# Performance work log

Hardware: AMD Instinct MI355X
Metric: run time of the kernel (lower is better)

## Reference

```python
import math
import jax, jax.numpy as jnp
import numpy as np

B, H, W, C = 4, 64, 64, 96
SSM_RATIO = 2.0
D_INNER = int(SSM_RATIO * C)   # 192
D_STATE = 4
DT_RANK = math.ceil(C / 16)    # 6
K = 4                          # 4 scan directions
D_CONV = 3


def layer_norm(x, g, b, eps=1e-5):
    mu = jnp.mean(x, axis=-1, keepdims=True)
    var = jnp.var(x, axis=-1, keepdims=True)
    return (x - mu) / jnp.sqrt(var + eps) * g + b


def cross_scan(x):
    # x: (B, D, H, W) -> (B, K=4, D, L); dirs: row-major, col-major, and their reverses
    b, d, h, w = x.shape
    s0 = x.reshape(b, d, h * w)
    s1 = jnp.transpose(x, (0, 1, 3, 2)).reshape(b, d, h * w)
    return jnp.stack([s0, s1, s0[..., ::-1], s1[..., ::-1]], axis=1)


def cross_merge(ys, h, w):
    # ys: (B, K=4, D, L) -> (B, D, L); inverse of cross_scan, summed over directions
    b, k, d, L = ys.shape
    ys = ys[:, 0:2] + ys[:, 2:4][..., ::-1]
    y0 = ys[:, 0]
    y1 = jnp.transpose(ys[:, 1].reshape(b, d, w, h), (0, 1, 3, 2)).reshape(b, d, L)
    return y0 + y1


def selective_scan(u, dt, A, Bm, Cm, D4):
    # u, dt: (B,K,D,L); A: (K,D,N); Bm, Cm: (B,K,N,L); D4: (K,D)
    u_l = jnp.moveaxis(u, -1, 0)    # (L,B,K,D)
    dt_l = jnp.moveaxis(dt, -1, 0)
    B_l = jnp.moveaxis(Bm, -1, 0)   # (L,B,K,N)
    C_l = jnp.moveaxis(Cm, -1, 0)

    def step(h, inp):
        u_t, dt_t, B_t, C_t = inp
        dA = jnp.exp(dt_t[..., None] * A)                              # (B,K,D,N)
        h = h * dA + dt_t[..., None] * B_t[:, :, None, :] * u_t[..., None]
        y = jnp.sum(h * C_t[:, :, None, :], axis=-1)                   # (B,K,D)
        return h, y

    h0 = jnp.zeros(u.shape[:3] + (A.shape[-1],), u.dtype)
    _, ys = jax.lax.scan(step, h0, (u_l, dt_l, B_l, C_l))
    return jnp.moveaxis(ys, 0, -1) + D4[None, :, :, None] * u


def _block(x_rgb, x_e, in_proj_x_w, in_proj_e_w, conv_x_w, conv_x_b, conv_e_w, conv_e_b,
           x_proj_weight, dt_projs_weight, dt_projs_bias, A_logs, Ds,
           ln_r_g, ln_r_b, ln_e_g, ln_e_b, out_proj_x_w, out_proj_e_w):
    b, h, w, c = x_rgb.shape
    Din, N, R = D_INNER, D_STATE, DT_RANK

    xr = jnp.einsum('bhwc,dc->bhwd', x_rgb, in_proj_x_w)
    xe = jnp.einsum('bhwc,dc->bhwd', x_e, in_proj_e_w)
    xr = jnp.transpose(xr, (0, 3, 1, 2))  # (B,Din,H,W)
    xe = jnp.transpose(xe, (0, 3, 1, 2))

    def dwconv(x, wt, bias):
        y = jax.lax.conv_general_dilated(x, wt, (1, 1), 'SAME', feature_group_count=Din)
        return jax.nn.silu(y + bias[None, :, None, None])

    xr = dwconv(xr, conv_x_w, conv_x_b)
    xe = dwconv(xe, conv_e_w, conv_e_b)

    xs_r = cross_scan(xr)  # (B,K,Din,L)
    xs_e = cross_scan(xe)

    def proj(xs):
        dbl = jnp.einsum('bkdl,kcd->bkcl', xs, x_proj_weight)
        dtl, Bm, Cm = dbl[:, :, :R], dbl[:, :, R:R + N], dbl[:, :, R + N:]
        dtl = jnp.einsum('bkrl,kdr->bkdl', dtl, dt_projs_weight)
        dtl = jax.nn.softplus(dtl + dt_projs_bias[None, :, :, None])
        return dtl, Bm, Cm

    dt_r, B_r, C_r = proj(xs_r)
    dt_e, B_e, C_e = proj(xs_e)

    A = -jnp.exp(A_logs).reshape(K, Din, N)
    D4 = Ds.reshape(K, Din)

    # cross fusion: each modality's scan reads out through the OTHER modality's C
    y_r = selective_scan(xs_r, dt_r, A, B_r, C_e, D4)
    y_e = selective_scan(xs_e, dt_e, A, B_e, C_r, D4)

    y_r = cross_merge(y_r, h, w)  # (B,Din,L)
    y_e = cross_merge(y_e, h, w)

    y_r = layer_norm(jnp.transpose(y_r, (0, 2, 1)), ln_r_g, ln_r_b).reshape(b, h, w, Din)
    y_e = layer_norm(jnp.transpose(y_e, (0, 2, 1)), ln_e_g, ln_e_b).reshape(b, h, w, Din)

    out_r = jnp.einsum('bhwd,cd->bhwc', y_r, out_proj_x_w)
    out_e = jnp.einsum('bhwd,cd->bhwc', y_e, out_proj_e_w)

    # residual add of the wrapping block (drop_path=0, mlp_ratio=0)
    return x_rgb + out_r, x_e + out_e


def setup_inputs():
    key = jax.random.key(0)
    ks = jax.random.split(key, 16)
    N, R, Din = D_STATE, DT_RANK, D_INNER

    def rn(k, shape, s=0.02):
        return (jax.random.normal(k, shape) * s).astype(jnp.float32)

    # dt bias: inverse-softplus of dt ~ U[1e-3, 0.1]  (mamba-style init)
    dt = jnp.exp(jax.random.uniform(ks[10], (K, Din)) * (np.log(0.1) - np.log(1e-3)) + np.log(1e-3))
    dt_bias = dt + jnp.log(-jnp.expm1(-dt))

    return {
        'x_rgb': jax.random.normal(ks[0], (B, H, W, C), jnp.float32),
        'x_e': jax.random.normal(ks[1], (B, H, W, C), jnp.float32),
        'in_proj_x_w': rn(ks[2], (Din, C)),
        'in_proj_e_w': rn(ks[3], (Din, C)),
        'conv_x_w': rn(ks[4], (Din, 1, D_CONV, D_CONV), 0.1),
        'conv_x_b': jnp.zeros((Din,), jnp.float32),
        'conv_e_w': rn(ks[5], (Din, 1, D_CONV, D_CONV), 0.1),
        'conv_e_b': jnp.zeros((Din,), jnp.float32),
        'x_proj_weight': rn(ks[6], (K, R + 2 * N, Din)),
        'dt_projs_weight': rn(ks[7], (K, Din, R), R ** -0.5),
        'dt_projs_bias': dt_bias.astype(jnp.float32),
        'A_logs': jnp.log(jnp.tile(jnp.arange(1, N + 1, dtype=jnp.float32), (K * Din, 1))),
        'Ds': jnp.ones((K * Din,), jnp.float32),
        'ln_r_g': jnp.ones((Din,), jnp.float32),
        'ln_r_b': jnp.zeros((Din,), jnp.float32),
        'ln_e_g': jnp.ones((Din,), jnp.float32),
        'ln_e_b': jnp.zeros((Din,), jnp.float32),
        'out_proj_x_w': rn(ks[8], (C, Din)),
        'out_proj_e_w': rn(ks[9], (C, Din)),
    }


def reference(x_rgb, x_e, in_proj_x_w, in_proj_e_w, conv_x_w, conv_x_b, conv_e_w, conv_e_b,
              x_proj_weight, dt_projs_weight, dt_projs_bias, A_logs, Ds,
              ln_r_g, ln_r_b, ln_e_g, ln_e_b, out_proj_x_w, out_proj_e_w):
    return _block(x_rgb, x_e, in_proj_x_w, in_proj_e_w, conv_x_w, conv_x_b, conv_e_w, conv_e_b,
                  x_proj_weight, dt_projs_weight, dt_projs_bias, A_logs, Ds,
                  ln_r_g, ln_r_b, ln_e_g, ln_e_b, out_proj_x_w, out_proj_e_w)
```

## Files before the change

kernel.cpp:

```cpp
#include <hip/hip_runtime.h>

#define BB 4
#define HH 64
#define WW 64
#define CC 96
#define DIN 192
#define NS 4
#define RR 6
#define KK 4
#define LL 4096
#define NPOS (BB*LL)
#define NPD ((size_t)NPOS*DIN)
#define NDBC ((size_t)BB*KK*LL*14)
#define NCHUNK 128
#define CLEN 32
#define NCHAIN 32
#define PB 16
#define TP 16

__device__ __forceinline__ int map_pos(int k, int l){
  switch(k){
    case 0: return l;
    case 1: { int wi=l>>6, hi=l&63; return hi*WW+wi; }
    case 2: return LL-1-l;
    default:{ int lr=LL-1-l; int wi=lr>>6, hi=lr&63; return hi*WW+wi; }
  }
}
__device__ __forceinline__ int pos_stride(int k){
  return (k==0) ? 1 : (k==1) ? WW : (k==2) ? -1 : -WW;
}

__global__ __launch_bounds__(DIN) void inproj_kernel(
    const float* __restrict__ x_rgb, const float* __restrict__ x_e,
    const float* __restrict__ w_r,   const float* __restrict__ w_e,
    float* __restrict__ xproj_r,    float* __restrict__ xproj_e){
  int blk = blockIdx.x;
  int m = blk / (NPOS/PB); int g = blk % (NPOS/PB);
  size_t rem0 = (size_t)g * PB;
  const float* x = m ? x_e : x_rgb;
  const float* w = m ? w_e : w_r;
  float* o = m ? xproj_e : xproj_r;
  __shared__ float4 xs4[PB*24];
  __shared__ float4 wt4[DIN*5];
  int t = threadIdx.x;

  const float4* xg = (const float4*)(x + rem0*CC);
  xs4[t]       = xg[t];
  xs4[t + 192] = xg[t + 192];

  float acc[PB];
  #pragma unroll
  for(int p=0;p<PB;p++) acc[p]=0.f;

  for(int c0=0; c0<CC; c0+=16){
    __syncthreads();
    const float* wr = w + (size_t)t*CC + c0;
    wt4[t*5+0] = *(const float4*)(wr);
    wt4[t*5+1] = *(const float4*)(wr+4);
    wt4[t*5+2] = *(const float4*)(wr+8);
    wt4[t*5+3] = *(const float4*)(wr+12);
    __syncthreads();
    int cq0 = c0 >> 2;
    #pragma unroll
    for(int q=0;q<4;q++){
      float4 w4 = wt4[t*5+q];
      #pragma unroll
      for(int p=0;p<PB;p++){
        float4 x4 = xs4[p*24 + cq0 + q];
        acc[p] = fmaf(x4.x,w4.x, fmaf(x4.y,w4.y, fmaf(x4.z,w4.z, fmaf(x4.w,w4.w, acc[p]))));
      }
    }
  }
  #pragma unroll
  for(int p=0;p<PB;p++) o[(rem0+p)*DIN + t] = acc[p];
}

__global__ __launch_bounds__(DIN) void conv_kernel(
    const float* __restrict__ xproj_r, const float* __restrict__ xproj_e,
    const float* __restrict__ cw_r, const float* __restrict__ cb_r,
    const float* __restrict__ cw_e, const float* __restrict__ cb_e,
    float* __restrict__ xconv_r, float* __restrict__ xconv_e){
  int blk = blockIdx.x;
  int m = blk / NPOS; int rem = blk % NPOS;
  int b = rem / LL, p = rem % LL;
  int y = p >> 6, x = p & 63;
  const float* in = (m ? xproj_e : xproj_r) + (size_t)b*LL*DIN;
  const float* cw = m ? cw_e : cw_r;
  const float* cb = m ? cb_e : cb_r;
  float* out = m ? xconv_e : xconv_r;
  int d = threadIdx.x;
  float acc = cb[d];
  #pragma unroll
  for(int dy=-1;dy<=1;dy++){
    int yy = y+dy; if(yy<0 || yy>=HH) continue;
    #pragma unroll
    for(int dx=-1;dx<=1;dx++){
      int xx = x+dx; if(xx<0 || xx>=WW) continue;
      acc += in[(size_t)(yy*WW+xx)*DIN + d] * cw[d*9 + (dy+1)*3 + (dx+1)];
    }
  }
  float s = acc / (1.f + __expf(-acc));
  out[(size_t)(b*LL+p)*DIN + d] = s;
}

#define TPOS 32
__global__ __launch_bounds__(256) void projbc_kernel(
    const float* __restrict__ xconv_r, const float* __restrict__ xconv_e,
    const float* __restrict__ xpw,
    float* __restrict__ dtBC_r, float* __restrict__ dtBC_e){
  int blk = blockIdx.x;
  int m = blk / (BB*LL/TPOS); int rem = blk % (BB*LL/TPOS);
  int b = rem / (LL/TPOS); int p0 = (rem % (LL/TPOS)) * TPOS;
  const float* xc = (m ? xconv_e : xconv_r) + ((size_t)b*LL + p0)*DIN;
  float* o = (m ? dtBC_e : dtBC_r) + (size_t)b*KK*LL*14;

  __shared__ float xs[TPOS*97];
  __shared__ float wsd[56*97];

  int t = threadIdx.x;
  int g = t >> 5;
  int pl = t & 31;

  float acc[7];
  #pragma unroll
  for(int j=0;j<7;j++) acc[j]=0.f;

  for(int dt0=0; dt0<DIN; dt0+=96){
    __syncthreads();
    for(int idx=t; idx<TPOS*96; idx+=256){
      int r = idx/96, ccol = idx%96;
      xs[r*97+ccol] = xc[(size_t)r*DIN + dt0 + ccol];
    }
    for(int idx=t; idx<56*96; idx+=256){
      int r = idx/96, ccol = idx%96;
      wsd[r*97+ccol] = xpw[(size_t)r*DIN + dt0 + ccol];
    }
    __syncthreads();
    const float* xrow = &xs[pl*97];
    #pragma unroll 4
    for(int d=0; d<96; d++){
      float xv = xrow[d];
      #pragma unroll
      for(int j=0;j<7;j++) acc[j] += wsd[(g*7+j)*97 + d]*xv;
    }
  }

  int p = p0 + pl;
  int ptr_ = (p&63)*64 + (p>>6);
  #pragma unroll
  for(int j=0;j<7;j++){
    int cbar = g*7+j;
    int k = cbar/14, c = cbar%14;
    int l = (k==0) ? p : (k==1) ? ptr_ : (k==2) ? (LL-1-p) : (LL-1-ptr_);
    o[((size_t)k*LL + l)*14 + c] = acc[j];
  }
}

__global__ __launch_bounds__(DIN) void scan_p1_kernel(
    const float* __restrict__ xconv_r, const float* __restrict__ xconv_e,
    const float* __restrict__ dtBC_r, const float* __restrict__ dtBC_e,
    const float* __restrict__ dtw, const float* __restrict__ dtb,
    const float* __restrict__ A_logs,
    float* __restrict__ trans_S, float* __restrict__ sumdt){
  int ch = blockIdx.x / NCHUNK;
  int cidx = blockIdx.x % NCHUNK;
  int m = ch >> 4, b = (ch>>2)&3, k = ch&3;
  int d = threadIdx.x;
  int l0 = cidx*CLEN;

  float4 al = *(const float4*)&A_logs[(size_t)(k*DIN+d)*NS];
  float A0=-__expf(al.x), A1=-__expf(al.y), A2=-__expf(al.z), A3=-__expf(al.w);
  float Wd[RR];
  #pragma unroll
  for(int r=0;r<RR;r++) Wd[r] = dtw[((size_t)k*DIN + d)*RR + r];
  float bias = dtb[k*DIN+d];

  const float* xc    = (m ? xconv_e : xconv_r) + (size_t)b*LL*DIN;
  const float* dbc_m = (m ? dtBC_e : dtBC_r) + ((size_t)b*KK + k)*LL*14;

  __shared__ float4 db4[CLEN][4];
  __shared__ float u_s[CLEN*DIN];
  float* dbf = (float*)db4;

  for(int idx=d; idx<CLEN*14; idx+=DIN){
    int i = idx/14, j = idx%14;
    int slot = (j<6) ? (8+j) : (j-6);
    dbf[i*16+slot] = dbc_m[(size_t)l0*14 + idx];
  }
  int stride = pos_stride(k);
  int pos0 = map_pos(k, l0);
  #pragma unroll 8
  for(int i=0;i<CLEN;i++)
    u_s[i*DIN+d] = xc[(size_t)(pos0+i*stride)*DIN + d];
  __syncthreads();

  float h0=0.f,h1=0.f,h2=0.f,h3=0.f,sd=0.f;
  #pragma unroll 4
  for(int i=0;i<CLEN;i++){
    float4 Bv  = db4[i][0];
    float4 d03 = db4[i][2];
    float4 d45 = db4[i][3];
    float dtr = fmaf(d03.x,Wd[0], fmaf(d03.y,Wd[1], fmaf(d03.z,Wd[2],
                fmaf(d03.w,Wd[3], fmaf(d45.x,Wd[4], fmaf(d45.y,Wd[5], bias))))));
    float dt = fmaxf(dtr,0.f) + __logf(1.f + __expf(-fabsf(dtr)));
    sd += dt;
    float u = u_s[i*DIN + d];
    float dtu = dt*u;
    h0 = fmaf(h0, __expf(dt*A0), dtu*Bv.x);
    h1 = fmaf(h1, __expf(dt*A1), dtu*Bv.y);
    h2 = fmaf(h2, __expf(dt*A2), dtu*Bv.z);
    h3 = fmaf(h3, __expf(dt*A3), dtu*Bv.w);
  }
  size_t base = ((size_t)(ch*NCHUNK + cidx)*NS)*DIN + d;
  trans_S[base          ] = h0;
  trans_S[base +   DIN  ] = h1;
  trans_S[base + 2*DIN  ] = h2;
  trans_S[base + 3*DIN  ] = h3;
  sumdt[(size_t)(ch*NCHUNK + cidx)*DIN + d] = sd;
}

__global__ __launch_bounds__(DIN) void scan_p2_kernel(
    const float* __restrict__ trans_S, const float* __restrict__ sumdt,
    const float* __restrict__ A_logs, float* __restrict__ hin){
  int ch = blockIdx.x; int k = ch & 3; int d = threadIdx.x;
  float4 al = *(const float4*)&A_logs[(size_t)(k*DIN+d)*NS];
  float A[NS] = {-__expf(al.x), -__expf(al.y), -__expf(al.z), -__expf(al.w)};
  float h[NS] = {0.f,0.f,0.f,0.f};
  for(int c0=0;c0<NCHUNK;c0+=4){
    float S[4][NS], sdv[4];
    #pragma unroll
    for(int cc=0;cc<4;cc++){
      size_t base = ((size_t)(ch*NCHUNK + c0+cc)*NS)*DIN + d;
      #pragma unroll
      for(int n=0;n<NS;n++) S[cc][n] = trans_S[base + (size_t)n*DIN];
      sdv[cc] = sumdt[(size_t)(ch*NCHUNK + c0+cc)*DIN + d];
    }
    #pragma unroll
    for(int cc=0;cc<4;cc++){
      size_t base = ((size_t)(ch*NCHUNK + c0+cc)*NS)*DIN + d;
      #pragma unroll
      for(int n=0;n<NS;n++) hin[base + (size_t)n*DIN] = h[n];
      #pragma unroll
      for(int n=0;n<NS;n++) h[n] = fmaf(h[n], __expf(A[n]*sdv[cc]), S[cc][n]);
    }
  }
}

__global__ __launch_bounds__(DIN) void scan_p3_kernel(
    const float* __restrict__ xconv_r, const float* __restrict__ xconv_e,
    const float* __restrict__ dtBC_r, const float* __restrict__ dtBC_e,
    const float* __restrict__ dtw, const float* __restrict__ dtb,
    const float* __restrict__ A_logs, const float* __restrict__ Ds,
    const float* __restrict__ hin,
    float* __restrict__ ym_a_r, float* __restrict__ ym_a_e,
    float* __restrict__ ym_b_r, float* __restrict__ ym_b_e){
  int blk = blockIdx.x;
  int cidx = blk % NCHUNK;
  int rem  = blk / NCHUNK;
  int pg = rem & 1; rem >>= 1;
  int b  = rem & 3; int m = rem >> 2;
  int kA = pg, kB = pg + 2;
  int cidx2 = NCHUNK-1-cidx;
  int l0A = cidx*CLEN, l0B = cidx2*CLEN;

  int d = threadIdx.x;
  int st = pos_stride(kA);
  int pos0 = map_pos(kA, l0A);

  const float* xc = (m ? xconv_e : xconv_r) + (size_t)b*LL*DIN;
  const float* dbc_own = (m ? dtBC_e : dtBC_r) + (size_t)b*KK*LL*14;
  const float* dbc_oth = (m ? dtBC_r : dtBC_e) + (size_t)b*KK*LL*14;
  float* ym = (pg==0) ? (m ? ym_a_e : ym_a_r) : (m ? ym_b_e : ym_b_r);
  ym += (size_t)b*LL*DIN;

  __shared__ float4 db4A[CLEN][4];
  __shared__ float4 db4B[CLEN][4];
  __shared__ float u_s[CLEN*DIN];
  float* dbfA = (float*)db4A;
  float* dbfB = (float*)db4B;

  for(int idx=d; idx<CLEN*14; idx+=DIN){
    int i = idx/14, j = idx%14;
    int slot = (j<6) ? (8+j) : (j-6);
    dbfA[i*16+slot] = dbc_own[((size_t)kA*LL + l0A)*14 + idx];
    dbfB[i*16+slot] = dbc_own[((size_t)kB*LL + l0B)*14 + idx];
  }
  for(int idx=d; idx<CLEN*NS; idx+=DIN){
    int i = idx>>2, j = idx&3;
    dbfA[i*16 + 4 + j] = dbc_oth[((size_t)kA*LL + l0A + i)*14 + 10 + j];
    dbfB[i*16 + 4 + j] = dbc_oth[((size_t)kB*LL + l0B + i)*14 + 10 + j];
  }
  #pragma unroll 8
  for(int i=0;i<CLEN;i++)
    u_s[i*DIN+d] = xc[(size_t)(pos0+i*st)*DIN + d];
  __syncthreads();

  {
    int k = kA;
    float4 al = *(const float4*)&A_logs[(size_t)(k*DIN+d)*NS];
    float A0=-__expf(al.x), A1=-__expf(al.y), A2=-__expf(al.z), A3=-__expf(al.w);
    float Wd[RR];
    #pragma unroll
    for(int r=0;r<RR;r++) Wd[r] = dtw[((size_t)k*DIN + d)*RR + r];
    float bias = dtb[k*DIN+d];
    float Dv = Ds[k*DIN+d];
    int chA = (m*4+b)*4 + kA;
    size_t hbase = ((size_t)(chA*NCHUNK + cidx)*NS)*DIN + d;
    float h0=hin[hbase], h1=hin[hbase+DIN], h2=hin[hbase+2*DIN], h3=hin[hbase+3*DIN];
    #pragma unroll 4
    for(int i=0;i<CLEN;i++){
      float4 Bv  = db4A[i][0];
      float4 Cv  = db4A[i][1];
      float4 d03 = db4A[i][2];
      float4 d45 = db4A[i][3];
      float dtr = fmaf(d03.x,Wd[0], fmaf(d03.y,Wd[1], fmaf(d03.z,Wd[2],
                  fmaf(d03.w,Wd[3], fmaf(d45.x,Wd[4], fmaf(d45.y,Wd[5], bias))))));
      float dt = fmaxf(dtr,0.f) + __logf(1.f + __expf(-fabsf(dtr)));
      float u = u_s[i*DIN + d];
      float dtu = dt*u;
      h0 = fmaf(h0, __expf(dt*A0), dtu*Bv.x);
      h1 = fmaf(h1, __expf(dt*A1), dtu*Bv.y);
      h2 = fmaf(h2, __expf(dt*A2), dtu*Bv.z);
      h3 = fmaf(h3, __expf(dt*A3), dtu*Bv.w);
      float y = fmaf(h0,Cv.x, fmaf(h1,Cv.y, fmaf(h2,Cv.z, fmaf(h3,Cv.w, Dv*u))));
      ym[(size_t)(pos0+i*st)*DIN + d] = y;
    }
  }
  {
    int k = kB;
    float4 al = *(const float4*)&A_logs[(size_t)(k*DIN+d)*NS];
    float A0=-__expf(al.x), A1=-__expf(al.y), A2=-__expf(al.z), A3=-__expf(al.w);
    float Wd[RR];
    #pragma unroll
    for(int r=0;r<RR;r++) Wd[r] = dtw[((size_t)k*DIN + d)*RR + r];
    float bias = dtb[k*DIN+d];
    float Dv = Ds[k*DIN+d];
    int chB = (m*4+b)*4 + kB;
    size_t hbase = ((size_t)(chB*NCHUNK + cidx2)*NS)*DIN + d;
    float h0=hin[hbase], h1=hin[hbase+DIN], h2=hin[hbase+2*DIN], h3=hin[hbase+3*DIN];
    #pragma unroll 4
    for(int j=0;j<CLEN;j++){
      int pi = CLEN-1-j;
      float4 Bv  = db4B[j][0];
      float4 Cv  = db4B[j][1];
      float4 d03 = db4B[j][2];
      float4 d45 = db4B[j][3];
      float dtr = fmaf(d03.x,Wd[0], fmaf(d03.y,Wd[1], fmaf(d03.z,Wd[2],
                  fmaf(d03.w,Wd[3], fmaf(d45.x,Wd[4], fmaf(d45.y,Wd[5], bias))))));
      float dt = fmaxf(dtr,0.f) + __logf(1.f + __expf(-fabsf(dtr)));
      float u = u_s[pi*DIN + d];
      float dtu = dt*u;
      h0 = fmaf(h0, __expf(dt*A0), dtu*Bv.x);
      h1 = fmaf(h1, __expf(dt*A1), dtu*Bv.y);
      h2 = fmaf(h2, __expf(dt*A2), dtu*Bv.z);
      h3 = fmaf(h3, __expf(dt*A3), dtu*Bv.w);
      float y = fmaf(h0,Cv.x, fmaf(h1,Cv.y, fmaf(h2,Cv.z, fmaf(h3,Cv.w, Dv*u))));
      size_t a = (size_t)(pos0+pi*st)*DIN + d;
      ym[a] += y;
    }
  }
}

__global__ __launch_bounds__(256) void ln_out_kernel(
    const float* __restrict__ ym_a_r, const float* __restrict__ ym_a_e,
    const float* __restrict__ ym_b_r, const float* __restrict__ ym_b_e,
    const float* __restrict__ ln_rg, const float* __restrict__ ln_rb,
    const float* __restrict__ ln_eg, const float* __restrict__ ln_eb,
    const float* __restrict__ opw_r, const float* __restrict__ opw_e,
    const float* __restrict__ x_rgb, const float* __restrict__ x_e,
    float* __restrict__ out){
  int blk = blockIdx.x;
  int m = blk / (NPOS/TP); int g = blk % (NPOS/TP);
  size_t rem0 = (size_t)g * TP;
  int t = threadIdx.x;

  __shared__ float yn_t[DIN][20];
  __shared__ float wt[CC][20];

  {
    int tp = t >> 4, j = t & 15;
    const float* yma = (m ? ym_a_e : ym_a_r) + (rem0+tp)*DIN;
    const float* ymb = (m ? ym_b_e : ym_b_r) + (rem0+tp)*DIN;
    float4 v4[3]; float s=0.f, q=0.f;
    #pragma unroll
    for(int e=0;e<3;e++){
      float4 a4 = *(const float4*)&yma[j*12 + e*4];
      float4 b4 = *(const float4*)&ymb[j*12 + e*4];
      v4[e] = make_float4(a4.x+b4.x, a4.y+b4.y, a4.z+b4.z, a4.w+b4.w);
      s += v4[e].x+v4[e].y+v4[e].z+v4[e].w;
      q += v4[e].x*v4[e].x + v4[e].y*v4[e].y + v4[e].z*v4[e].z + v4[e].w*v4[e].w;
    }
    #pragma unroll
    for(int off=8; off>0; off>>=1){ s += __shfl_xor(s,off); q += __shfl_xor(q,off); }
    float mu  = s*(1.f/DIN);
    float var = q*(1.f/DIN) - mu*mu;
    float inv = rsqrtf(var + 1e-5f);
    const float* gg = m ? ln_eg : ln_rg;
    const float* be = m ? ln_eb : ln_rb;
    #pragma unroll
    for(int e=0;e<3;e++){
      int dd = j*12 + e*4;
      float4 g4 = *(const float4*)&gg[dd];
      float4 b4 = *(const float4*)&be[dd];
      yn_t[dd+0][tp] = (v4[e].x-mu)*inv*g4.x + b4.x;
      yn_t[dd+1][tp] = (v4[e].y-mu)*inv*g4.y + b4.y;
      yn_t[dd+2][tp] = (v4[e].z-mu)*inv*g4.z + b4.z;
      yn_t[dd+3][tp] = (v4[e].w-mu)*inv*g4.w + b4.w;
    }
  }

  int c = t % CC;
  int pbase = t / CC;
  const float* w = (m ? opw_e : opw_r);
  float acc[8];
  #pragma unroll
  for(int pp=0;pp<8;pp++) acc[pp]=0.f;

  for(int d0=0; d0<DIN; d0+=16){
    __syncthreads();
    for(int idx=t; idx<CC*16; idx+=256){
      int r = idx>>4, cc2 = idx&15;
      wt[r][cc2] = w[(size_t)r*DIN + d0 + cc2];
    }
    __syncthreads();
    if(t < 192){
      #pragma unroll
      for(int q4=0; q4<4; q4++){
        float4 w4 = *(const float4*)&wt[c][q4*4];
        #pragma unroll
        for(int e=0;e<4;e++){
          int dd = d0 + q4*4 + e;
          float wv = (e==0)?w4.x:(e==1)?w4.y:(e==2)?w4.z:w4.w;
          float4 ylo = *(const float4*)&yn_t[dd][pbase*8];
          float4 yhi = *(const float4*)&yn_t[dd][pbase*8+4];
          acc[0] = fmaf(ylo.x, wv, acc[0]);
          acc[1] = fmaf(ylo.y, wv, acc[1]);
          acc[2] = fmaf(ylo.z, wv, acc[2]);
          acc[3] = fmaf(ylo.w, wv, acc[3]);
          acc[4] = fmaf(yhi.x, wv, acc[4]);
          acc[5] = fmaf(yhi.y, wv, acc[5]);
          acc[6] = fmaf(yhi.z, wv, acc[6]);
          acc[7] = fmaf(yhi.w, wv, acc[7]);
        }
      }
    }
  }
  if(t < 192){
    const float* xin = m ? x_e : x_rgb;
    #pragma unroll
    for(int pp=0;pp<8;pp++){
      size_t rem = rem0 + pbase*8 + pp;
      size_t oi = (size_t)m*NPOS*CC + rem*CC + c;
      out[oi] = acc[pp] + xin[rem*CC + c];
    }
  }
}

extern "C" void kernel_launch(void* const* d_in, const int* in_sizes, int n_in,
                              void* d_out, int out_size, void* d_ws, size_t ws_size,
                              hipStream_t stream){
  const float* x_rgb = (const float*)d_in[0];
  const float* x_e   = (const float*)d_in[1];
  const float* ipw_r = (const float*)d_in[2];
  const float* ipw_e = (const float*)d_in[3];
  const float* cw_r  = (const float*)d_in[4];
  const float* cb_r  = (const float*)d_in[5];
  const float* cw_e  = (const float*)d_in[6];
  const float* cb_e  = (const float*)d_in[7];
  const float* xpw   = (const float*)d_in[8];
  const float* dtw   = (const float*)d_in[9];
  const float* dtb   = (const float*)d_in[10];
  const float* Alog  = (const float*)d_in[11];
  const float* Ds_   = (const float*)d_in[12];
  const float* ln_rg = (const float*)d_in[13];
  const float* ln_rb = (const float*)d_in[14];
  const float* ln_eg = (const float*)d_in[15];
  const float* ln_eb = (const float*)d_in[16];
  const float* opw_r = (const float*)d_in[17];
  const float* opw_e = (const float*)d_in[18];
  float* out = (float*)d_out;

  float* ws = (float*)d_ws;
  float* xproj_r = ws;
  float* xproj_e = ws + NPD;
  float* xconv_r = ws + 2*NPD;
  float* xconv_e = ws + 3*NPD;
  float* dtBC_r  = ws + 4*NPD;
  float* dtBC_e  = ws + 4*NPD + NDBC;
  float* trans_S = ws + 4*NPD + 2*NDBC;
  float* sumdt   = trans_S + (size_t)NCHAIN*NCHUNK*NS*DIN;
  float* hin     = sumdt   + (size_t)NCHAIN*NCHUNK*DIN;
  float* ym_b_r  = hin     + (size_t)NCHAIN*NCHUNK*NS*DIN;
  float* ym_b_e  = ym_b_r + NPD;
  float* ym_a_r = xproj_r;
  float* ym_a_e = xproj_e;

  inproj_kernel<<<2*NPOS/PB, DIN, 0, stream>>>(x_rgb, x_e, ipw_r, ipw_e, xproj_r, xproj_e);
  conv_kernel<<<2*NPOS, DIN, 0, stream>>>(xproj_r, xproj_e, cw_r, cb_r, cw_e, cb_e, xconv_r, xconv_e);
  projbc_kernel<<<2*BB*(LL/TPOS), 256, 0, stream>>>(xconv_r, xconv_e, xpw, dtBC_r, dtBC_e);
  scan_p1_kernel<<<NCHAIN*NCHUNK, DIN, 0, stream>>>(xconv_r, xconv_e, dtBC_r, dtBC_e,
                                                    dtw, dtb, Alog, trans_S, sumdt);
  scan_p2_kernel<<<NCHAIN, DIN, 0, stream>>>(trans_S, sumdt, Alog, hin);
  scan_p3_kernel<<<2*BB*2*NCHUNK, DIN, 0, stream>>>(xconv_r, xconv_e, dtBC_r, dtBC_e,
                                                    dtw, dtb, Alog, Ds_, hin,
                                                    ym_a_r, ym_a_e, ym_b_r, ym_b_e);
  ln_out_kernel<<<2*NPOS/TP, 256, 0, stream>>>(ym_a_r, ym_a_e, ym_b_r, ym_b_e,
                                               ln_rg, ln_rb, ln_eg, ln_eb,
                                               opw_r, opw_e, x_rgb, x_e, out);
}
```

Before: 373.0 us.

## Pair forward/reverse scan directions in pass 1, buffer outputs, widen LN-out tile

Scan pass 1 now handles a direction and its reverse in one block, so the u chunk is loaded from global memory once for both. This halves the block count and the redundant xconv reads. Scan pass 3 keeps the forward outputs in a fully unrolled register array and writes each ym element once, removing the read-modify-write accumulation. The LayerNorm/out-projection kernel now processes 32 positions per block with 16 accumulators per thread, so weight tiles are reused more. The cost is higher register pressure (a 32-float array plus 16 accumulators), which may reduce occupancy.

Result: slower. 381.6 us (+2.3%).

```diff
diff --git a/kernel.cpp b/kernel.cpp
--- a/kernel.cpp
+++ b/kernel.cpp
@@ -16,7 +16,7 @@
 #define CLEN 32
 #define NCHAIN 32
 #define PB 16
-#define TP 16
+#define TP 32
 
 __device__ __forceinline__ int map_pos(int k, int l){
   switch(k){
@@ -162,61 +162,105 @@
     const float* __restrict__ dtw, const float* __restrict__ dtb,
     const float* __restrict__ A_logs,
     float* __restrict__ trans_S, float* __restrict__ sumdt){
-  int ch = blockIdx.x / NCHUNK;
-  int cidx = blockIdx.x % NCHUNK;
-  int m = ch >> 4, b = (ch>>2)&3, k = ch&3;
+  int blk = blockIdx.x;
+  int cidx = blk % NCHUNK;
+  int rem  = blk / NCHUNK;
+  int pg = rem & 1; rem >>= 1;
+  int b  = rem & 3; int m = rem >> 2;
+  int kA = pg, kB = pg + 2;
+  int cidx2 = NCHUNK-1-cidx;
+  int l0A = cidx*CLEN, l0B = cidx2*CLEN;
   int d = threadIdx.x;
-  int l0 = cidx*CLEN;
-
-  float4 al = *(const float4*)&A_logs[(size_t)(k*DIN+d)*NS];
-  float A0=-__expf(al.x), A1=-__expf(al.y), A2=-__expf(al.z), A3=-__expf(al.w);
-  float Wd[RR];
-  #pragma unroll
-  for(int r=0;r<RR;r++) Wd[r] = dtw[((size_t)k*DIN + d)*RR + r];
-  float bias = dtb[k*DIN+d];
-
-  const float* xc    = (m ? xconv_e : xconv_r) + (size_t)b*LL*DIN;
-  const float* dbc_m = (m ? dtBC_e : dtBC_r) + ((size_t)b*KK + k)*LL*14;
-
-  __shared__ float4 db4[CLEN][4];
+  int st = pos_stride(kA);
+  int pos0 = map_pos(kA, l0A);
+
+  const float* xc = (m ? xconv_e : xconv_r) + (size_t)b*LL*DIN;
+  const float* dbc_own = (m ? dtBC_e : dtBC_r) + (size_t)b*KK*LL*14;
+
+  __shared__ float4 db4A[CLEN][4];
+  __shared__ float4 db4B[CLEN][4];
   __shared__ float u_s[CLEN*DIN];
-  float* dbf = (float*)db4;
+  float* dbfA = (float*)db4A;
+  float* dbfB = (float*)db4B;
 
   for(int idx=d; idx<CLEN*14; idx+=DIN){
     int i = idx/14, j = idx%14;
     int slot = (j<6) ? (8+j) : (j-6);
-    dbf[i*16+slot] = dbc_m[(size_t)l0*14 + idx];
-  }
-  int stride = pos_stride(k);
-  int pos0 = map_pos(k, l0);
+    dbfA[i*16+slot] = dbc_own[((size_t)kA*LL + l0A)*14 + idx];
+    dbfB[i*16+slot] = dbc_own[((size_t)kB*LL + l0B)*14 + idx];
+  }
   #pragma unroll 8
   for(int i=0;i<CLEN;i++)
-    u_s[i*DIN+d] = xc[(size_t)(pos0+i*stride)*DIN + d];
+    u_s[i*DIN+d] = xc[(size_t)(pos0+i*st)*DIN + d];
   __syncthreads();
 
-  float h0=0.f,h1=0.f,h2=0.f,h3=0.f,sd=0.f;
-  #pragma unroll 4
-  for(int i=0;i<CLEN;i++){
-    float4 Bv  = db4[i][0];
-    float4 d03 = db4[i][2];
-    float4 d45 = db4[i][3];
-    float dtr = fmaf(d03.x,Wd[0], fmaf(d03.y,Wd[1], fmaf(d03.z,Wd[2],
-                fmaf(d03.w,Wd[3], fmaf(d45.x,Wd[4], fmaf(d45.y,Wd[5], bias))))));
-    float dt = fmaxf(dtr,0.f) + __logf(1.f + __expf(-fabsf(dtr)));
-    sd += dt;
-    float u = u_s[i*DIN + d];
-    float dtu = dt*u;
-    h0 = fmaf(h0, __expf(dt*A0), dtu*Bv.x);
-    h1 = fmaf(h1, __expf(dt*A1), dtu*Bv.y);
-    h2 = fmaf(h2, __expf(dt*A2), dtu*Bv.z);
-    h3 = fmaf(h3, __expf(dt*A3), dtu*Bv.w);
-  }
-  size_t base = ((size_t)(ch*NCHUNK + cidx)*NS)*DIN + d;
-  trans_S[base          ] = h0;
-  trans_S[base +   DIN  ] = h1;
-  trans_S[base + 2*DIN  ] = h2;
-  trans_S[base + 3*DIN  ] = h3;
-  sumdt[(size_t)(ch*NCHUNK + cidx)*DIN + d] = sd;
+  {
+    int k = kA;
+    float4 al = *(const float4*)&A_logs[(size_t)(k*DIN+d)*NS];
+    float A0=-__expf(al.x), A1=-__expf(al.y), A2=-__expf(al.z), A3=-__expf(al.w);
+    float Wd[RR];
+    #pragma unroll
+    for(int r=0;r<RR;r++) Wd[r] = dtw[((size_t)k*DIN + d)*RR + r];
+    float bias = dtb[k*DIN+d];
+    float h0=0.f,h1=0.f,h2=0.f,h3=0.f,sd=0.f;
+    #pragma unroll 4
+    for(int i=0;i<CLEN;i++){
+      float4 Bv  = db4A[i][0];
+      float4 d03 = db4A[i][2];
+      float4 d45 = db4A[i][3];
+      float dtr = fmaf(d03.x,Wd[0], fmaf(d03.y,Wd[1], fmaf(d03.z,Wd[2],
+                  fmaf(d03.w,Wd[3], fmaf(d45.x,Wd[4], fmaf(d45.y,Wd[5], bias))))));
+      float dt = fmaxf(dtr,0.f) + __logf(1.f + __expf(-fabsf(dtr)));
+      sd += dt;
+      float u = u_s[i*DIN + d];
+      float dtu = dt*u;
+      h0 = fmaf(h0, __expf(dt*A0), dtu*Bv.x);
+      h1 = fmaf(h1, __expf(dt*A1), dtu*Bv.y);
+      h2 = fmaf(h2, __expf(dt*A2), dtu*Bv.z);
+      h3 = fmaf(h3, __expf(dt*A3), dtu*Bv.w);
+    }
+    int chA = (m*4+b)*4 + kA;
+    size_t base = ((size_t)(chA*NCHUNK + cidx)*NS)*DIN + d;
+    trans_S[base        ] = h0;
+    trans_S[base +  DIN ] = h1;
+    trans_S[base + 2*DIN] = h2;
+    trans_S[base + 3*DIN] = h3;
+    sumdt[(size_t)(chA*NCHUNK + cidx)*DIN + d] = sd;
+  }
+  {
+    int k = kB;
+    float4 al = *(const float4*)&A_logs[(size_t)(k*DIN+d)*NS];
+    float A0=-__expf(al.x), A1=-__expf(al.y), A2=-__expf(al.z), A3=-__expf(al.w);
+    float Wd[RR];
+    #pragma unroll
+    for(int r=0;r<RR;r++) Wd[r] = dtw[((size_t)k*DIN + d)*RR + r];
+    float bias = dtb[k*DIN+d];
+    float h0=0.f,h1=0.f,h2=0.f,h3=0.f,sd=0.f;
+    #pragma unroll 4
+    for(int j=0;j<CLEN;j++){
+      int pi = CLEN-1-j;
+      float4 Bv  = db4B[j][0];
+      float4 d03 = db4B[j][2];
+      float4 d45 = db4B[j][3];
+      float dtr = fmaf(d03.x,Wd[0], fmaf(d03.y,Wd[1], fmaf(d03.z,Wd[2],
+                  fmaf(d03.w,Wd[3], fmaf(d45.x,Wd[4], fmaf(d45.y,Wd[5], bias))))));
+      float dt = fmaxf(dtr,0.f) + __logf(1.f + __expf(-fabsf(dtr)));
+      sd += dt;
+      float u = u_s[pi*DIN + d];
+      float dtu = dt*u;
+      h0 = fmaf(h0, __expf(dt*A0), dtu*Bv.x);
+      h1 = fmaf(h1, __expf(dt*A1), dtu*Bv.y);
+      h2 = fmaf(h2, __expf(dt*A2), dtu*Bv.z);
+      h3 = fmaf(h3, __expf(dt*A3), dtu*Bv.w);
+    }
+    int chB = (m*4+b)*4 + kB;
+    size_t base = ((size_t)(chB*NCHUNK + cidx2)*NS)*DIN + d;
+    trans_S[base        ] = h0;
+    trans_S[base +  DIN ] = h1;
+    trans_S[base + 2*DIN] = h2;
+    trans_S[base + 3*DIN] = h3;
+    sumdt[(size_t)(chB*NCHUNK + cidx2)*DIN + d] = sd;
+  }
 }
 
 __global__ __launch_bounds__(DIN) void scan_p2_kernel(
@@ -295,6 +339,8 @@
     u_s[i*DIN+d] = xc[(size_t)(pos0+i*st)*DIN + d];
   __syncthreads();
 
+  float yA[CLEN];
+
   {
     int k = kA;
     float4 al = *(const float4*)&A_logs[(size_t)(k*DIN+d)*NS];
@@ -307,7 +353,7 @@
     int chA = (m*4+b)*4 + kA;
     size_t hbase = ((size_t)(chA*NCHUNK + cidx)*NS)*DIN + d;
     float h0=hin[hbase], h1=hin[hbase+DIN], h2=hin[hbase+2*DIN], h3=hin[hbase+3*DIN];
-    #pragma unroll 4
+    #pragma unroll
     for(int i=0;i<CLEN;i++){
       float4 Bv  = db4A[i][0];
       float4 Cv  = db4A[i][1];
@@ -322,8 +368,7 @@
       h1 = fmaf(h1, __expf(dt*A1), dtu*Bv.y);
       h2 = fmaf(h2, __expf(dt*A2), dtu*Bv.z);
       h3 = fmaf(h3, __expf(dt*A3), dtu*Bv.w);
-      float y = fmaf(h0,Cv.x, fmaf(h1,Cv.y, fmaf(h2,Cv.z, fmaf(h3,Cv.w, Dv*u))));
-      ym[(size_t)(pos0+i*st)*DIN + d] = y;
+      yA[i] = fmaf(h0,Cv.x, fmaf(h1,Cv.y, fmaf(h2,Cv.z, fmaf(h3,Cv.w, Dv*u))));
     }
   }
   {
@@ -338,7 +383,7 @@
     int chB = (m*4+b)*4 + kB;
     size_t hbase = ((size_t)(chB*NCHUNK + cidx2)*NS)*DIN + d;
     float h0=hin[hbase], h1=hin[hbase+DIN], h2=hin[hbase+2*DIN], h3=hin[hbase+3*DIN];
-    #pragma unroll 4
+    #pragma unroll
     for(int j=0;j<CLEN;j++){
       int pi = CLEN-1-j;
       float4 Bv  = db4B[j][0];
@@ -355,8 +400,7 @@
       h2 = fmaf(h2, __expf(dt*A2), dtu*Bv.z);
       h3 = fmaf(h3, __expf(dt*A3), dtu*Bv.w);
       float y = fmaf(h0,Cv.x, fmaf(h1,Cv.y, fmaf(h2,Cv.z, fmaf(h3,Cv.w, Dv*u))));
-      size_t a = (size_t)(pos0+pi*st)*DIN + d;
-      ym[a] += y;
+      ym[(size_t)(pos0+pi*st)*DIN + d] = yA[pi] + y;
     }
   }
 }
@@ -374,32 +418,33 @@
   size_t rem0 = (size_t)g * TP;
   int t = threadIdx.x;
 
-  __shared__ float yn_t[DIN][20];
+  __shared__ float yn_t[DIN][36];
   __shared__ float wt[CC][20];
 
   {
-    int tp = t >> 4, j = t & 15;
+    int tp = t >> 3, j = t & 7;
     const float* yma = (m ? ym_a_e : ym_a_r) + (rem0+tp)*DIN;
     const float* ymb = (m ? ym_b_e : ym_b_r) + (rem0+tp)*DIN;
-    float4 v4[3]; float s=0.f, q=0.f;
-    #pragma unroll
-    for(int e=0;e<3;e++){
-      float4 a4 = *(const float4*)&yma[j*12 + e*4];
-      float4 b4 = *(const float4*)&ymb[j*12 + e*4];
+    float4 v4[6]; float s=0.f, q=0.f;
+    #pragma unroll
+    for(int e=0;e<6;e++){
+      int dd = j*4 + e*32;
+      float4 a4 = *(const float4*)&yma[dd];
+      float4 b4 = *(const float4*)&ymb[dd];
       v4[e] = make_float4(a4.x+b4.x, a4.y+b4.y, a4.z+b4.z, a4.w+b4.w);
       s += v4[e].x+v4[e].y+v4[e].z+v4[e].w;
       q += v4[e].x*v4[e].x + v4[e].y*v4[e].y + v4[e].z*v4[e].z + v4[e].w*v4[e].w;
     }
     #pragma unroll
-    for(int off=8; off>0; off>>=1){ s += __shfl_xor(s,off); q += __shfl_xor(q,off); }
+    for(int off=4; off>0; off>>=1){ s += __shfl_xor(s,off); q += __shfl_xor(q,off); }
     float mu  = s*(1.f/DIN);
     float var = q*(1.f/DIN) - mu*mu;
     float inv = rsqrtf(var + 1e-5f);
     const float* gg = m ? ln_eg : ln_rg;
     const float* be = m ? ln_eb : ln_rb;
     #pragma unroll
-    for(int e=0;e<3;e++){
-      int dd = j*12 + e*4;
+    for(int e=0;e<6;e++){
+      int dd = j*4 + e*32;
       float4 g4 = *(const float4*)&gg[dd];
       float4 b4 = *(const float4*)&be[dd];
       yn_t[dd+0][tp] = (v4[e].x-mu)*inv*g4.x + b4.x;
@@ -412,9 +457,9 @@
   int c = t % CC;
   int pbase = t / CC;
   const float* w = (m ? opw_e : opw_r);
-  float acc[8];
+  float acc[16];
   #pragma unroll
-  for(int pp=0;pp<8;pp++) acc[pp]=0.f;
+  for(int pp=0;pp<16;pp++) acc[pp]=0.f;
 
   for(int d0=0; d0<DIN; d0+=16){
     __syncthreads();
@@ -431,16 +476,26 @@
         for(int e=0;e<4;e++){
           int dd = d0 + q4*4 + e;
           float wv = (e==0)?w4.x:(e==1)?w4.y:(e==2)?w4.z:w4.w;
-          float4 ylo = *(const float4*)&yn_t[dd][pbase*8];
-          float4 yhi = *(const float4*)&yn_t[dd][pbase*8+4];
-          acc[0] = fmaf(ylo.x, wv, acc[0]);
-          acc[1] = fmaf(ylo.y, wv, acc[1]);
-          acc[2] = fmaf(ylo.z, wv, acc[2]);
-          acc[3] = fmaf(ylo.w, wv, acc[3]);
-          acc[4] = fmaf(yhi.x, wv, acc[4]);
-          acc[5] = fmaf(yhi.y, wv, acc[5]);
-          acc[6] = fmaf(yhi.z, wv, acc[6]);
-          acc[7] = fmaf(yhi.w, wv, acc[7]);
+          float4 y0 = *(const float4*)&yn_t[dd][pbase*16];
+          float4 y1 = *(const float4*)&yn_t[dd][pbase*16+4];
+          float4 y2 = *(const float4*)&yn_t[dd][pbase*16+8];
+          float4 y3 = *(const float4*)&yn_t[dd][pbase*16+12];
+          acc[ 0] = fmaf(y0.x, wv, acc[ 0]);
+          acc[ 1] = fmaf(y0.y, wv, acc[ 1]);
+          acc[ 2] = fmaf(y0.z, wv, acc[ 2]);
+          acc[ 3] = fmaf(y0.w, wv, acc[ 3]);
+          acc[ 4] = fmaf(y1.x, wv, acc[ 4]);
+          acc[ 5] = fmaf(y1.y, wv, acc[ 5]);
+          acc[ 6] = fmaf(y1.z, wv, acc[ 6]);
+          acc[ 7] = fmaf(y1.w, wv, acc[ 7]);
+          acc[ 8] = fmaf(y2.x, wv, acc[ 8]);
+          acc[ 9] = fmaf(y2.y, wv, acc[ 9]);
+          acc[10] = fmaf(y2.z, wv, acc[10]);
+          acc[11] = fmaf(y2.w, wv, acc[11]);
+          acc[12] = fmaf(y3.x, wv, acc[12]);
+          acc[13] = fmaf(y3.y, wv, acc[13]);
+          acc[14] = fmaf(y3.z, wv, acc[14]);
+          acc[15] = fmaf(y3.w, wv, acc[15]);
         }
       }
     }
@@ -448,8 +503,8 @@
   if(t < 192){
     const float* xin = m ? x_e : x_rgb;
     #pragma unroll
-    for(int pp=0;pp<8;pp++){
-      size_t rem = rem0 + pbase*8 + pp;
+    for(int pp=0;pp<16;pp++){
+      size_t rem = rem0 + pbase*16 + pp;
       size_t oi = (size_t)m*NPOS*CC + rem*CC + c;
       out[oi] = acc[pp] + xin[rem*CC + c];
     }
@@ -498,7 +553,7 @@
   inproj_kernel<<<2*NPOS/PB, DIN, 0, stream>>>(x_rgb, x_e, ipw_r, ipw_e, xproj_r, xproj_e);
   conv_kernel<<<2*NPOS, DIN, 0, stream>>>(xproj_r, xproj_e, cw_r, cb_r, cw_e, cb_e, xconv_r, xconv_e);
   projbc_kernel<<<2*BB*(LL/TPOS), 256, 0, stream>>>(xconv_r, xconv_e, xpw, dtBC_r, dtBC_e);
-  scan_p1_kernel<<<NCHAIN*NCHUNK, DIN, 0, stream>>>(xconv_r, xconv_e, dtBC_r, dtBC_e,
+  scan_p1_kernel<<<2*BB*2*NCHUNK, DIN, 0, stream>>>(xconv_r, xconv_e, dtBC_r, dtBC_e,
                                                     dtw, dtb, Alog, trans_S, sumdt);
   scan_p2_kernel<<<NCHAIN, DIN, 0, stream>>>(trans_S, sumdt, Alog, hin);
   scan_p3_kernel<<<2*BB*2*NCHUNK, DIN, 0, stream>>>(xconv_r, xconv_e, dtBC_r, dtBC_e,
```
